# Optimization experiments

Measured on AMD Instinct MI355X. Metric: run time of the kernel, lower is better.

## Reference

```python
import jax, jax.numpy as jnp
import numpy as np

H = 16        # num_attention_heads
G = 16        # groups
SCALE_MIN = 0.95
SCALE_MAX = 1.05


def setup_inputs() -> dict:
    key = jax.random.key(0)
    ks = jax.random.split(key, 9)
    B, S, E = 2, 2048, 1024
    d = {
        'hidden_states': jax.random.normal(ks[0], (B, S, E), jnp.float32),
        'Wq': jax.random.normal(ks[1], (E, E), jnp.float32) * (E ** -0.5),
        'bq': jax.random.normal(ks[2], (E,), jnp.float32) * 0.02,
        'Wk': jax.random.normal(ks[3], (E, E), jnp.float32) * (E ** -0.5),
        'bk': jax.random.normal(ks[4], (E,), jnp.float32) * 0.02,
        'Wv': jax.random.normal(ks[5], (E, E), jnp.float32) * (E ** -0.5),
        'bv': jax.random.normal(ks[6], (E,), jnp.float32) * 0.02,
        'Ws': jax.random.normal(ks[7], (H * G, E), jnp.float32) * (E ** -0.5),
        'bs': jax.random.normal(ks[8], (H * G,), jnp.float32) * 0.02,
    }
    return d


def _shape_heads(x, B, S):
    # [B,S,h*D] -> [B,h,S,D]
    return x.reshape(B, S, H, -1).transpose(0, 2, 1, 3)


def reference(hidden_states, Wq, bq, Wk, bk, Wv, bv, Ws, bs):
    B, S, E = hidden_states.shape
    D = E // H            # head dim = 64
    gd = D // G           # group dim = 4

    Q = _shape_heads(hidden_states @ Wq.T + bq, B, S)   # [B,h,S,D]
    K = _shape_heads(hidden_states @ Wk.T + bk, B, S)
    V = _shape_heads(hidden_states @ Wv.T + bv, B, S)

    # groupwise dynamic scales, narrow sigmoid range
    s_logits = hidden_states @ Ws.T + bs                 # [B,S,h*g]
    s = jax.nn.sigmoid(s_logits) * (SCALE_MAX - SCALE_MIN) + SCALE_MIN
    s = s.reshape(B, S, H, G).transpose(0, 2, 1, 3)      # [B,h,S,g]
    s = jnp.repeat(s, gd, axis=-1)                       # [B,h,S,D]

    Q = Q * s  # apply_to='q'

    scores = jnp.einsum('bhsd,bhtd->bhst', Q, K) / jnp.sqrt(jnp.float32(D))
    probs = jax.nn.softmax(scores, axis=-1)
    ctx = jnp.einsum('bhst,bhtd->bhsd', probs, V)        # [B,h,S,D]
    ctx = ctx.transpose(0, 2, 1, 3).reshape(B, S, H * D)
    return ctx
```

## Files before the change

kernel.cpp:

```cpp
#include <hip/hip_runtime.h>

typedef short bf16x8 __attribute__((ext_vector_type(8)));
typedef float f32x4 __attribute__((ext_vector_type(4)));

__device__ inline float bf2f(ushort u) {
    unsigned v = ((unsigned)u) << 16;
    return __builtin_bit_cast(float, v);
}
__device__ inline ushort f2bf(float f) {
    unsigned u = __builtin_bit_cast(unsigned, f);
    u += 0x7fffu + ((u >> 16) & 1u);
    return (ushort)(u >> 16);
}
__device__ inline void async_load16(const ushort* g, ushort* l) {
    __builtin_amdgcn_global_load_lds((const __attribute__((address_space(1))) void*)g,
                                     (__attribute__((address_space(3))) void*)l, 16, 0, 0);
}

__global__ void cast_f32_bf16(const float* __restrict__ src, ushort* __restrict__ dst, int n) {
    int i = (blockIdx.x * 256 + threadIdx.x) * 8;
    if (i >= n) return;
    float4 a = *(const float4*)(src + i);
    float4 b = *(const float4*)(src + i + 4);
    union { ushort u[8]; float4 v; } o;
    o.u[0] = f2bf(a.x); o.u[1] = f2bf(a.y); o.u[2] = f2bf(a.z); o.u[3] = f2bf(a.w);
    o.u[4] = f2bf(b.x); o.u[5] = f2bf(b.y); o.u[6] = f2bf(b.z); o.u[7] = f2bf(b.w);
    *(float4*)(dst + i) = o.v;
}

__launch_bounds__(256, 3)
__global__ void fused_qkvs(const ushort* __restrict__ X,
                           const ushort* __restrict__ Wq, const ushort* __restrict__ Wk,
                           const ushort* __restrict__ Wv, const ushort* __restrict__ Ws,
                           const float* __restrict__ bq, const float* __restrict__ bk,
                           const float* __restrict__ bv, const float* __restrict__ bs,
                           ushort* __restrict__ Qb, ushort* __restrict__ Kb,
                           ushort* __restrict__ VtG, float* __restrict__ sb)
{
    __shared__ __align__(16) ushort Sm[128 * 136];
    ushort* As = Sm;
    ushort* Bs = Sm + 128 * 64;

    const int tid = threadIdx.x, w = tid >> 6, lane = tid & 63;
    const int l15 = lane & 15, quad = lane >> 4;
    const int lrow = lane >> 3;
    const int gchunk = ((lane & 7) ^ lrow) * 8;

    const int wid = blockIdx.x;
    const int r8 = wid & 7, jj = wid >> 3;
    const int by = (jj & 3) * 8 + r8;
    const int xb = jj >> 2;
    const int m0 = by * 128;

    const ushort* W; const float* bias; int n0, mode;
    if (xb < 8)       { W = Wq; bias = bq; n0 = xb * 128;        mode = 1; }
    else if (xb < 16) { W = Wk; bias = bk; n0 = (xb - 8) * 128;  mode = 0; }
    else if (xb < 24) { W = Wv; bias = bv; n0 = (xb - 16) * 128; mode = 2; }
    else              { W = Ws; bias = bs; n0 = (xb - 24) * 128; mode = 3; }

    const int wm = (w >> 1) * 64, wn = (w & 1) * 64;

    f32x4 acc[4][4];
    for (int i = 0; i < 4; i++) for (int j = 0; j < 4; j++) acc[i][j] = (f32x4){0.f, 0.f, 0.f, 0.f};

    for (int k0 = 0; k0 < 1024; k0 += 64) {
        __syncthreads();
        for (int c = 0; c < 4; ++c) {
            int r = w * 32 + c * 8;
            async_load16(&X[(size_t)(m0 + r + lrow) * 1024 + k0 + gchunk], &As[r * 64]);
            async_load16(&W[(size_t)(n0 + r + lrow) * 1024 + k0 + gchunk], &Bs[r * 64]);
        }
        __syncthreads();
        for (int kk = 0; kk < 64; kk += 32) {
            const int csw = quad + (kk >> 3);
            bf16x8 a[4], b[4];
            for (int i = 0; i < 4; i++)
                a[i] = *(const bf16x8*)&As[(wm + i * 16 + l15) * 64 + ((csw ^ (l15 & 7)) * 8)];
            for (int j = 0; j < 4; j++)
                b[j] = *(const bf16x8*)&Bs[(wn + j * 16 + l15) * 64 + ((csw ^ (l15 & 7)) * 8)];
            for (int i = 0; i < 4; i++)
                for (int j = 0; j < 4; j++)
                    acc[i][j] = __builtin_amdgcn_mfma_f32_16x16x32_bf16(a[i], b[j], acc[i][j], 0, 0, 0);
        }
    }

    const float QSCALE = 0.125f * 1.44269504f;

    if (mode == 3) {
        for (int i = 0; i < 4; i++)
            for (int j = 0; j < 4; j++) {
                int gn = n0 + wn + j * 16 + l15;
                float bv_ = bias[gn];
                for (int r = 0; r < 4; r++) {
                    int gm = m0 + wm + i * 16 + quad * 4 + r;
                    float v = acc[i][j][r] + bv_;
                    float sg = 1.0f / (1.0f + exp2f(-v * 1.44269504f));
                    sb[(size_t)gm * 256 + gn] = sg * 0.1f + 0.95f;
                }
            }
        return;
    }

    __syncthreads();

    if (mode == 2) {
        for (int i = 0; i < 4; i++)
            for (int j = 0; j < 4; j++) {
                int gnl = wn + j * 16 + l15;
                float bv_ = bias[n0 + gnl];
                ushort4 pk;
                pk.x = f2bf(acc[i][j][0] + bv_);
                pk.y = f2bf(acc[i][j][1] + bv_);
                pk.z = f2bf(acc[i][j][2] + bv_);
                pk.w = f2bf(acc[i][j][3] + bv_);
                *(ushort4*)&Sm[gnl * 136 + wm + i * 16 + quad * 4] = pk;
            }
        __syncthreads();
        const int bb = m0 >> 11, sloc = m0 & 2047;
        for (int it = 0; it < 8; ++it) {
            int d = (tid >> 4) + it * 16;
            int s8 = (tid & 15) * 8;
            float4 v = *(float4*)&Sm[d * 136 + s8];
            int h = (n0 + d) >> 6, dd = d & 63;
            *(float4*)&VtG[(size_t)(bb * 16 + h) * 131072 + (size_t)dd * 2048 + sloc + s8] = v;
        }
    } else {
        for (int i = 0; i < 4; i++)
            for (int j = 0; j < 4; j++) {
                int gnl = wn + j * 16 + l15;
                float bv_ = bias[n0 + gnl];
                for (int r = 0; r < 4; r++) {
                    float v = acc[i][j][r] + bv_;
                    if (mode == 1) v *= QSCALE;
                    Sm[(wm + i * 16 + quad * 4 + r) * 136 + gnl] = f2bf(v);
                }
            }
        __syncthreads();
        ushort* dst = (mode == 1) ? Qb : Kb;
        for (int it = 0; it < 8; ++it) {
            int row = (tid >> 4) + it * 16, c = (tid & 15) * 8;
            *(float4*)&dst[(size_t)(m0 + row) * 1024 + n0 + c] = *(float4*)&Sm[row * 136 + c];
        }
    }
}

__launch_bounds__(256, 2)
__global__ void attn_kernel(const ushort* __restrict__ Q, const ushort* __restrict__ K,
                            const ushort* __restrict__ Vt, const float* __restrict__ sb,
                            float* __restrict__ out)
{
    __shared__ __align__(16) ushort Qs[128 * 72];
    __shared__ __align__(16) ushort Ps[128 * 72];
    __shared__ __align__(16) ushort Ks0[64 * 64];
    __shared__ __align__(16) ushort Ks1[64 * 64];
    __shared__ __align__(16) ushort Vs0[64 * 64];
    __shared__ __align__(16) ushort Vs1[64 * 64];

    const int tid = threadIdx.x, w = tid >> 6, lane = tid & 63;
    const int l15 = lane & 15, quad = lane >> 4;
    const int lrow = lane >> 3;
    const int gchunk = ((lane & 7) ^ lrow) * 8;

    const int wid = blockIdx.x;
    const int r8 = wid & 7, jj = wid >> 3;
    const int bh = (jj & 3) * 8 + r8;
    const int qx = jj >> 2;
    const int b = bh >> 4, h = bh & 15;
    const int q0 = qx * 128;
    const size_t rowbase = (size_t)b * 2048;
    const int cbase = h * 64;

    for (int it = 0; it < 4; ++it) {
        int l = tid + it * 256;
        int r = l >> 3, c = (l & 7) * 8;
        union { float4 f; ushort u[8]; } uu, oo;
        uu.f = *(const float4*)&Q[(rowbase + q0 + r) * 1024 + cbase + c];
        const float* sp = &sb[(rowbase + q0 + r) * 256 + ((cbase + c) >> 2)];
        float s0 = sp[0], s1 = sp[1];
        for (int j = 0; j < 4; j++) oo.u[j] = f2bf(bf2f(uu.u[j]) * s0);
        for (int j = 4; j < 8; j++) oo.u[j] = f2bf(bf2f(uu.u[j]) * s1);
        *(float4*)&Qs[r * 72 + c] = oo.f;
    }

    for (int c = 0; c < 2; ++c) {
        int r = w * 16 + c * 8;
        async_load16(&K[(rowbase + r + lrow) * 1024 + cbase + gchunk], &Ks0[r * 64]);
        async_load16(&Vt[(size_t)bh * 131072 + (size_t)(r + lrow) * 2048 + gchunk], &Vs0[r * 64]);
    }

    float lsum[2][4];
    f32x4 o[2][4];
    for (int mt = 0; mt < 2; mt++) for (int r = 0; r < 4; r++) lsum[mt][r] = 0.f;
    for (int mt = 0; mt < 2; mt++) for (int nt = 0; nt < 4; nt++) o[mt][nt] = (f32x4){0.f, 0.f, 0.f, 0.f};

#define ATTN_STEP(KC, VC, KN, VN, KT, PREFETCH)                                                         \
    {                                                                                                   \
        __syncthreads();                \
        if (PREFETCH) {                                                                                 \
            int nk = (KT) + 1;                                                                          \
            for (int c = 0; c < 2; ++c) {                                                               \
                int r = w * 16 + c * 8;                                                                 \
                async_load16(&K[(rowbase + nk * 64 + r + lrow) * 1024 + cbase + gchunk], &KN[r * 64]);  \
                async_load16(&Vt[(size_t)bh * 131072 + (size_t)(r + lrow) * 2048 + nk * 64 + gchunk],   \
                             &VN[r * 64]);                                                              \
            }                                                                                           \
        }                                                                                               \
        f32x4 sacc[2][4];                                                                               \
        for (int mt = 0; mt < 2; mt++)                                                                  \
            for (int nt = 0; nt < 4; nt++) sacc[mt][nt] = (f32x4){0.f, 0.f, 0.f, 0.f};                  \
        for (int kk = 0; kk < 64; kk += 32) {                                                           \
            const int csw = ((quad + (kk >> 3)) ^ (l15 & 7)) * 8;                                       \
            bf16x8 a[2], bb[4];                                                                         \
            for (int mt = 0; mt < 2; mt++)                                                              \
                a[mt] = *(const bf16x8*)&Qs[(w * 32 + mt * 16 + l15) * 72 + kk + quad * 8];             \
            for (int nt = 0; nt < 4; nt++)                                                              \
                bb[nt] = *(const bf16x8*)&KC[(nt * 16 + l15) * 64 + csw];                               \
            for (int mt = 0; mt < 2; mt++)                                                              \
                for (int nt = 0; nt < 4; nt++)                                                          \
                    sacc[mt][nt] = __builtin_amdgcn_mfma_f32_16x16x32_bf16(a[mt], bb[nt],               \
                                                                           sacc[mt][nt], 0, 0, 0);     \
        }                                                                                               \
        for (int mt = 0; mt < 2; mt++)                                                                  \
            for (int nt = 0; nt < 4; nt++)                                                              \
                for (int r = 0; r < 4; r++) {                                                           \
                    float p = exp2f(sacc[mt][nt][r]);                                                   \
                    lsum[mt][r] += p;                                                                   \
                    Ps[(w * 32 + mt * 16 + quad * 4 + r) * 72 + nt * 16 + l15] = f2bf(p);               \
                }                                                                                       \
                           \
        for (int kk = 0; kk < 64; kk += 32) {                                                           \
            const int csw = ((quad + (kk >> 3)) ^ (l15 & 7)) * 8;                                       \
            bf16x8 a[2], bb[4];                                                                         \
            for (int mt = 0; mt < 2; mt++)                                                              \
                a[mt] = *(const bf16x8*)&Ps[(w * 32 + mt * 16 + l15) * 72 + kk + quad * 8];             \
            for (int nt = 0; nt < 4; nt++)                                                              \
                bb[nt] = *(const bf16x8*)&VC[(nt * 16 + l15) * 64 + csw];                               \
            for (int mt = 0; mt < 2; mt++)                                                              \
                for (int nt = 0; nt < 4; nt++)                                                          \
                    o[mt][nt] = __builtin_amdgcn_mfma_f32_16x16x32_bf16(a[mt], bb[nt],                  \
                                                                        o[mt][nt], 0, 0, 0);            \
        }                                                                                               \
    }

    for (int kt = 0; kt < 32; kt += 2) {
        ATTN_STEP(Ks0, Vs0, Ks1, Vs1, kt, 1);
        ATTN_STEP(Ks1, Vs1, Ks0, Vs0, kt + 1, (kt + 2 < 32));
    }
#undef ATTN_STEP

    for (int mt = 0; mt < 2; mt++)
        for (int r = 0; r < 4; r++) {
            float s = lsum[mt][r];
            for (int off = 1; off < 16; off <<= 1) s += __shfl_xor(s, off);
            lsum[mt][r] = s;
        }

    for (int mt = 0; mt < 2; mt++) {
        for (int r = 0; r < 4; r++) {
            float inv = 1.0f / lsum[mt][r];
            int q = q0 + w * 32 + mt * 16 + quad * 4 + r;
            size_t base = (rowbase + q) * 1024 + cbase;
            for (int nt = 0; nt < 4; nt++)
                out[base + nt * 16 + l15] = o[mt][nt][r] * inv;
        }
    }
}

extern "C" void kernel_launch(void* const* d_in, const int* in_sizes, int n_in,
                              void* d_out, int out_size, void* d_ws, size_t ws_size,
                              hipStream_t stream) {
    const float* hs = (const float*)d_in[0];
    const float* Wq = (const float*)d_in[1];
    const float* bq = (const float*)d_in[2];
    const float* Wk = (const float*)d_in[3];
    const float* bk = (const float*)d_in[4];
    const float* Wv = (const float*)d_in[5];
    const float* bv = (const float*)d_in[6];
    const float* Ws = (const float*)d_in[7];
    const float* bs = (const float*)d_in[8];
    float* outp = (float*)d_out;

    char* ws = (char*)d_ws;
    ushort* Qb    = (ushort*)(ws);
    ushort* Kb    = (ushort*)(ws + 8388608);
    ushort* VtG   = (ushort*)(ws + 16777216);
    float*  sb    = (float* )(ws + 25165824);
    ushort* hs_bf = (ushort*)(ws + 29360128);
    ushort* Wq_bf = (ushort*)(ws + 37748736);
    ushort* Wk_bf = (ushort*)(ws + 39845888);
    ushort* Wv_bf = (ushort*)(ws + 41943040);
    ushort* Ws_bf = (ushort*)(ws + 44040192);

    dim3 blk(256);
    cast_f32_bf16<<<dim3(2048), blk, 0, stream>>>(hs, hs_bf, 4194304);
    cast_f32_bf16<<<dim3(512),  blk, 0, stream>>>(Wq, Wq_bf, 1048576);
    cast_f32_bf16<<<dim3(512),  blk, 0, stream>>>(Wk, Wk_bf, 1048576);
    cast_f32_bf16<<<dim3(512),  blk, 0, stream>>>(Wv, Wv_bf, 1048576);
    cast_f32_bf16<<<dim3(128),  blk, 0, stream>>>(Ws, Ws_bf, 262144);

    fused_qkvs<<<dim3(832), blk, 0, stream>>>(hs_bf, Wq_bf, Wk_bf, Wv_bf, Ws_bf,
                                              bq, bk, bv, bs, Qb, Kb, VtG, sb);
    attn_kernel<<<dim3(512), blk, 0, stream>>>(Qb, Kb, VtG, sb, outp);
}
```

Measured before the change: 208.5 us.

## Load K/V fragments directly from global, merge casts, raise occupancy bounds

```diff
diff --git a/kernel.cpp b/kernel.cpp
--- a/kernel.cpp
+++ b/kernel.cpp
@@ -17,9 +17,21 @@
                                      (__attribute__((address_space(3))) void*)l, 16, 0, 0);
 }
 
-__global__ void cast_f32_bf16(const float* __restrict__ src, ushort* __restrict__ dst, int n) {
-    int i = (blockIdx.x * 256 + threadIdx.x) * 8;
-    if (i >= n) return;
+__global__ void cast_all(const float* __restrict__ hs, const float* __restrict__ Wq,
+                         const float* __restrict__ Wk, const float* __restrict__ Wv,
+                         const float* __restrict__ Ws,
+                         ushort* __restrict__ dhs, ushort* __restrict__ dWq,
+                         ushort* __restrict__ dWk, ushort* __restrict__ dWv,
+                         ushort* __restrict__ dWs)
+{
+    int bid = blockIdx.x;
+    const float* src; ushort* dst; int off;
+    if (bid < 2048)      { src = hs; dst = dhs; off = bid; }
+    else if (bid < 2560) { src = Wq; dst = dWq; off = bid - 2048; }
+    else if (bid < 3072) { src = Wk; dst = dWk; off = bid - 2560; }
+    else if (bid < 3584) { src = Wv; dst = dWv; off = bid - 3072; }
+    else                 { src = Ws; dst = dWs; off = bid - 3584; }
+    int i = (off * 256 + threadIdx.x) * 8;
     float4 a = *(const float4*)(src + i);
     float4 b = *(const float4*)(src + i + 4);
     union { ushort u[8]; float4 v; } o;
@@ -28,7 +40,7 @@
     *(float4*)(dst + i) = o.v;
 }
 
-__launch_bounds__(256, 3)
+__launch_bounds__(256, 4)
 __global__ void fused_qkvs(const ushort* __restrict__ X,
                            const ushort* __restrict__ Wq, const ushort* __restrict__ Wk,
                            const ushort* __restrict__ Wv, const ushort* __restrict__ Ws,
@@ -144,22 +156,16 @@
     }
 }
 
-__launch_bounds__(256, 2)
+__launch_bounds__(256, 3)
 __global__ void attn_kernel(const ushort* __restrict__ Q, const ushort* __restrict__ K,
                             const ushort* __restrict__ Vt, const float* __restrict__ sb,
                             float* __restrict__ out)
 {
     __shared__ __align__(16) ushort Qs[128 * 72];
     __shared__ __align__(16) ushort Ps[128 * 72];
-    __shared__ __align__(16) ushort Ks0[64 * 64];
-    __shared__ __align__(16) ushort Ks1[64 * 64];
-    __shared__ __align__(16) ushort Vs0[64 * 64];
-    __shared__ __align__(16) ushort Vs1[64 * 64];
 
     const int tid = threadIdx.x, w = tid >> 6, lane = tid & 63;
     const int l15 = lane & 15, quad = lane >> 4;
-    const int lrow = lane >> 3;
-    const int gchunk = ((lane & 7) ^ lrow) * 8;
 
     const int wid = blockIdx.x;
     const int r8 = wid & 7, jj = wid >> 3;
@@ -181,72 +187,58 @@
         for (int j = 4; j < 8; j++) oo.u[j] = f2bf(bf2f(uu.u[j]) * s1);
         *(float4*)&Qs[r * 72 + c] = oo.f;
     }
-
-    for (int c = 0; c < 2; ++c) {
-        int r = w * 16 + c * 8;
-        async_load16(&K[(rowbase + r + lrow) * 1024 + cbase + gchunk], &Ks0[r * 64]);
-        async_load16(&Vt[(size_t)bh * 131072 + (size_t)(r + lrow) * 2048 + gchunk], &Vs0[r * 64]);
-    }
+    __syncthreads();
+
+    bf16x8 aq[2][2];
+    for (int mt = 0; mt < 2; mt++)
+        for (int kk2 = 0; kk2 < 2; kk2++)
+            aq[mt][kk2] = *(const bf16x8*)&Qs[(w * 32 + mt * 16 + l15) * 72 + kk2 * 32 + quad * 8];
+
+    const ushort* Kbase = K + rowbase * 1024 + cbase;
+    const ushort* Vbase = Vt + (size_t)bh * 131072;
 
     float lsum[2][4];
     f32x4 o[2][4];
     for (int mt = 0; mt < 2; mt++) for (int r = 0; r < 4; r++) lsum[mt][r] = 0.f;
     for (int mt = 0; mt < 2; mt++) for (int nt = 0; nt < 4; nt++) o[mt][nt] = (f32x4){0.f, 0.f, 0.f, 0.f};
 
-#define ATTN_STEP(KC, VC, KN, VN, KT, PREFETCH)                                                         \
-    {                                                                                                   \
-        __syncthreads();                \
-        if (PREFETCH) {                                                                                 \
-            int nk = (KT) + 1;                                                                          \
-            for (int c = 0; c < 2; ++c) {                                                               \
-                int r = w * 16 + c * 8;                                                                 \
-                async_load16(&K[(rowbase + nk * 64 + r + lrow) * 1024 + cbase + gchunk], &KN[r * 64]);  \
-                async_load16(&Vt[(size_t)bh * 131072 + (size_t)(r + lrow) * 2048 + nk * 64 + gchunk],   \
-                             &VN[r * 64]);                                                              \
-            }                                                                                           \
-        }                                                                                               \
-        f32x4 sacc[2][4];                                                                               \
-        for (int mt = 0; mt < 2; mt++)                                                                  \
-            for (int nt = 0; nt < 4; nt++) sacc[mt][nt] = (f32x4){0.f, 0.f, 0.f, 0.f};                  \
-        for (int kk = 0; kk < 64; kk += 32) {                                                           \
-            const int csw = ((quad + (kk >> 3)) ^ (l15 & 7)) * 8;                                       \
-            bf16x8 a[2], bb[4];                                                                         \
-            for (int mt = 0; mt < 2; mt++)                                                              \
-                a[mt] = *(const bf16x8*)&Qs[(w * 32 + mt * 16 + l15) * 72 + kk + quad * 8];             \
-            for (int nt = 0; nt < 4; nt++)                                                              \
-                bb[nt] = *(const bf16x8*)&KC[(nt * 16 + l15) * 64 + csw];                               \
-            for (int mt = 0; mt < 2; mt++)                                                              \
-                for (int nt = 0; nt < 4; nt++)                                                          \
-                    sacc[mt][nt] = __builtin_amdgcn_mfma_f32_16x16x32_bf16(a[mt], bb[nt],               \
-                                                                           sacc[mt][nt], 0, 0, 0);     \
-        }                                                                                               \
-        for (int mt = 0; mt < 2; mt++)                                                                  \
-            for (int nt = 0; nt < 4; nt++)                                                              \
-                for (int r = 0; r < 4; r++) {                                                           \
-                    float p = exp2f(sacc[mt][nt][r]);                                                   \
-                    lsum[mt][r] += p;                                                                   \
-                    Ps[(w * 32 + mt * 16 + quad * 4 + r) * 72 + nt * 16 + l15] = f2bf(p);               \
-                }                                                                                       \
-                           \
-        for (int kk = 0; kk < 64; kk += 32) {                                                           \
-            const int csw = ((quad + (kk >> 3)) ^ (l15 & 7)) * 8;                                       \
-            bf16x8 a[2], bb[4];                                                                         \
-            for (int mt = 0; mt < 2; mt++)                                                              \
-                a[mt] = *(const bf16x8*)&Ps[(w * 32 + mt * 16 + l15) * 72 + kk + quad * 8];             \
-            for (int nt = 0; nt < 4; nt++)                                                              \
-                bb[nt] = *(const bf16x8*)&VC[(nt * 16 + l15) * 64 + csw];                               \
-            for (int mt = 0; mt < 2; mt++)                                                              \
-                for (int nt = 0; nt < 4; nt++)                                                          \
-                    o[mt][nt] = __builtin_amdgcn_mfma_f32_16x16x32_bf16(a[mt], bb[nt],                  \
-                                                                        o[mt][nt], 0, 0, 0);            \
-        }                                                                                               \
-    }
-
-    for (int kt = 0; kt < 32; kt += 2) {
-        ATTN_STEP(Ks0, Vs0, Ks1, Vs1, kt, 1);
-        ATTN_STEP(Ks1, Vs1, Ks0, Vs0, kt + 1, (kt + 2 < 32));
-    }
-#undef ATTN_STEP
+    for (int kt = 0; kt < 32; ++kt) {
+        const int k0 = kt * 64;
+
+        bf16x8 kb[2][4], vb[2][4];
+        for (int kk2 = 0; kk2 < 2; kk2++)
+            for (int nt = 0; nt < 4; nt++) {
+                kb[kk2][nt] = *(const bf16x8*)&Kbase[(size_t)(k0 + nt * 16 + l15) * 1024 + kk2 * 32 + quad * 8];
+                vb[kk2][nt] = *(const bf16x8*)&Vbase[(size_t)(nt * 16 + l15) * 2048 + k0 + kk2 * 32 + quad * 8];
+            }
+
+        f32x4 sacc[2][4];
+        for (int mt = 0; mt < 2; mt++)
+            for (int nt = 0; nt < 4; nt++) sacc[mt][nt] = (f32x4){0.f, 0.f, 0.f, 0.f};
+        for (int kk2 = 0; kk2 < 2; kk2++)
+            for (int mt = 0; mt < 2; mt++)
+                for (int nt = 0; nt < 4; nt++)
+                    sacc[mt][nt] = __builtin_amdgcn_mfma_f32_16x16x32_bf16(aq[mt][kk2], kb[kk2][nt],
+                                                                           sacc[mt][nt], 0, 0, 0);
+
+        for (int mt = 0; mt < 2; mt++)
+            for (int nt = 0; nt < 4; nt++)
+                for (int r = 0; r < 4; r++) {
+                    float p = exp2f(sacc[mt][nt][r]);
+                    lsum[mt][r] += p;
+                    Ps[(w * 32 + mt * 16 + quad * 4 + r) * 72 + nt * 16 + l15] = f2bf(p);
+                }
+
+        for (int kk2 = 0; kk2 < 2; kk2++) {
+            bf16x8 a[2];
+            for (int mt = 0; mt < 2; mt++)
+                a[mt] = *(const bf16x8*)&Ps[(w * 32 + mt * 16 + l15) * 72 + kk2 * 32 + quad * 8];
+            for (int mt = 0; mt < 2; mt++)
+                for (int nt = 0; nt < 4; nt++)
+                    o[mt][nt] = __builtin_amdgcn_mfma_f32_16x16x32_bf16(a[mt], vb[kk2][nt],
+                                                                        o[mt][nt], 0, 0, 0);
+        }
+    }
 
     for (int mt = 0; mt < 2; mt++)
         for (int r = 0; r < 4; r++) {
@@ -292,12 +284,8 @@
     ushort* Ws_bf = (ushort*)(ws + 44040192);
 
     dim3 blk(256);
-    cast_f32_bf16<<<dim3(2048), blk, 0, stream>>>(hs, hs_bf, 4194304);
-    cast_f32_bf16<<<dim3(512),  blk, 0, stream>>>(Wq, Wq_bf, 1048576);
-    cast_f32_bf16<<<dim3(512),  blk, 0, stream>>>(Wk, Wk_bf, 1048576);
-    cast_f32_bf16<<<dim3(512),  blk, 0, stream>>>(Wv, Wv_bf, 1048576);
-    cast_f32_bf16<<<dim3(128),  blk, 0, stream>>>(Ws, Ws_bf, 262144);
-
+    cast_all<<<dim3(3712), blk, 0, stream>>>(hs, Wq, Wk, Wv, Ws,
+                                             hs_bf, Wq_bf, Wk_bf, Wv_bf, Ws_bf);
     fused_qkvs<<<dim3(832), blk, 0, stream>>>(hs_bf, Wq_bf, Wk_bf, Wv_bf, Ws_bf,
                                               bq, bk, bv, bs, Qb, Kb, VtG, sb);
     attn_kernel<<<dim3(512), blk, 0, stream>>>(Qb, Kb, VtG, sb, outp);
```

After: 282.0 us. 1.35x slower.
